# Kernel tuning notes

Hardware: AMD Instinct MI355X
Metric: run time of the kernel (lower is better)

The kernel has to match this reference:

```python
import jax, jax.numpy as jnp
import numpy as np

MAX_REL_POS = 16


def relative_position_ids(t, max_pos):
    r = jnp.arange(t)
    dist = jnp.clip(r[None, :] - r[:, None], -max_pos, max_pos)
    return dist + max_pos  # [T, T] in [0, 2*max_pos]


def setup_inputs():
    key = jax.random.key(0)
    ks = jax.random.split(key, 5)
    B, H, T, D = 2, 16, 1024, 64
    V = 2 * MAX_REL_POS + 1  # 33
    q = jax.random.normal(ks[0], (B, H, T, D), dtype=jnp.float32)
    k = jax.random.normal(ks[1], (B, H, T, D), dtype=jnp.float32)
    v = jax.random.normal(ks[2], (B, H, T, D), dtype=jnp.float32)
    embed_k = jax.random.normal(ks[3], (V, D), dtype=jnp.float32)
    embed_v = jax.random.normal(ks[4], (V, D), dtype=jnp.float32)
    mask = jnp.zeros((1, 1, T, T), dtype=jnp.float32)
    return {"q": q, "k": k, "v": v, "embed_k": embed_k, "embed_v": embed_v, "mask": mask}


def reference(q, k, v, embed_k, embed_v, mask):
    T = q.shape[2]
    D = k.shape[-1]
    rel = relative_position_ids(T, MAX_REL_POS)           # [T, T] int
    rel_k = embed_k[rel]                                   # [T, T, D]
    rel_v = embed_v[rel]                                   # [T, T, D]
    # QK^T plus relative-key term (matmul_with_relative_representations, transpose_b=True)
    logits = jnp.einsum('bhqd,bhkd->bhqk', q, k) + jnp.einsum('bhqd,qkd->bhqk', q, rel_k)
    logits = logits * (1.0 / jnp.sqrt(jnp.asarray(D, dtype=logits.dtype)))
    logits = logits + mask * (-1e9)
    attn = jax.nn.softmax(logits, axis=-1)                 # [B, H, T, T]
    out = jnp.einsum('bhqk,bhkd->bhqd', attn, v) + jnp.einsum('bhqk,qkd->bhqd', attn, rel_v)
    return out, attn
```

## Files before the change

### kernel.cpp

```cpp
#include <hip/hip_runtime.h>

#define BHN 32
#define T 1024
#define DD 64
#define TQ 16
#define PST 1032

typedef __attribute__((ext_vector_type(8))) __bf16 bf16x8;
typedef __attribute__((ext_vector_type(8))) unsigned short us8;
typedef __attribute__((ext_vector_type(4))) float f32x4;

struct alignas(16) U4 { unsigned a, b, c, d; };

__device__ __forceinline__ unsigned short f2bf(float x) {
  unsigned u = __builtin_bit_cast(unsigned, x);
  u += 0x7fffu + ((u >> 16) & 1u);
  return (unsigned short)(u >> 16);
}
__device__ __forceinline__ float bf2f(unsigned short h) {
  unsigned u = ((unsigned)h) << 16;
  return __builtin_bit_cast(float, u);
}
__device__ __forceinline__ bf16x8 ld_bf16x8(const unsigned short* p) {
  U4 u = *(const U4*)p;
  return __builtin_bit_cast(bf16x8, u);
}

__global__ __launch_bounds__(256) void prep_conv(
    const float* __restrict__ k, const float* __restrict__ v,
    unsigned short* __restrict__ kbf, unsigned short* __restrict__ vt)
{
  __shared__ float sT[64][65];
  const int bh = blockIdx.y;
  const int tb = blockIdx.x * 64;
  const int t = threadIdx.x;
  const size_t base = (size_t)bh * T * DD + (size_t)tb * DD;

  const float4* ksrc = (const float4*)(k + base);
  ushort4* kdst = (ushort4*)(kbf + base);
#pragma unroll
  for (int i = 0; i < 4; ++i) {
    int g = i * 256 + t;
    float4 f = ksrc[g];
    ushort4 u;
    u.x = f2bf(f.x); u.y = f2bf(f.y); u.z = f2bf(f.z); u.w = f2bf(f.w);
    kdst[g] = u;
  }

  const float* vsrc = v + base;
#pragma unroll
  for (int i = 0; i < 16; ++i) {
    int e = i * 256 + t;
    sT[e & 63][e >> 6] = vsrc[e];
  }
  __syncthreads();
  unsigned short* vdst = vt + (size_t)bh * DD * T + tb;
#pragma unroll
  for (int i = 0; i < 16; ++i) {
    int e = i * 256 + t;
    int dd = e >> 6, kk = e & 63;
    vdst[(size_t)dd * T + kk] = f2bf(sT[dd][kk]);
  }
}

__global__ __launch_bounds__(256, 4) void attn_main(
    const float* __restrict__ q, const unsigned short* __restrict__ kbf,
    const unsigned short* __restrict__ vt, const float* __restrict__ ek,
    const float* __restrict__ ev, const float* __restrict__ mask,
    float* __restrict__ out, float* __restrict__ attn)
{
  __shared__ unsigned short sP[TQ * PST];
  __shared__ float sQek[TQ][33];
  __shared__ float sDiag[TQ][31];
  __shared__ float sRS[4][TQ];
  __shared__ float sRB[4][TQ];
  __shared__ float sInv[TQ];
  __shared__ float sB0n[TQ];

  const int bh = blockIdx.y;
  const int qb = blockIdx.x * TQ;
  const int tid = threadIdx.x;
  const int wave = tid >> 6;
  const int lane = tid & 63;
  const int quad = lane >> 4;
  const int col = lane & 15;

  for (int i = tid; i < TQ * 31; i += 256) (&sDiag[0][0])[i] = 0.f;

  const float* qrows = q + (size_t)bh * T * DD + (size_t)qb * DD;
  for (int idx = tid; idx < TQ * 33; idx += 256) {
    int i = idx / 33;
    int r = idx - i * 33;
    const float4* qa = (const float4*)(qrows + i * DD);
    const float4* eb = (const float4*)(ek + r * DD);
    float acc = 0.f;
#pragma unroll
    for (int d4 = 0; d4 < 16; ++d4) {
      float4 a = qa[d4], b = eb[d4];
      acc += a.x * b.x + a.y * b.y + a.z * b.z + a.w * b.w;
    }
    sQek[i][r] = acc;
  }
  __syncthreads();

  bf16x8 aq0, aq1;
  {
    const float* qp = qrows + col * DD + quad * 8;
    float4 f0 = *(const float4*)(qp);
    float4 f1 = *(const float4*)(qp + 4);
    float4 f2 = *(const float4*)(qp + 32);
    float4 f3 = *(const float4*)(qp + 36);
    us8 u0, u1;
    u0[0] = f2bf(f0.x); u0[1] = f2bf(f0.y); u0[2] = f2bf(f0.z); u0[3] = f2bf(f0.w);
    u0[4] = f2bf(f1.x); u0[5] = f2bf(f1.y); u0[6] = f2bf(f1.z); u0[7] = f2bf(f1.w);
    u1[0] = f2bf(f2.x); u1[1] = f2bf(f2.y); u1[2] = f2bf(f2.z); u1[3] = f2bf(f2.w);
    u1[4] = f2bf(f3.x); u1[5] = f2bf(f3.y); u1[6] = f2bf(f3.z); u1[7] = f2bf(f3.w);
    aq0 = __builtin_bit_cast(bf16x8, u0);
    aq1 = __builtin_bit_cast(bf16x8, u1);
  }

  float regS[4] = {0.f, 0.f, 0.f, 0.f};
  float regB[4] = {0.f, 0.f, 0.f, 0.f};
  const unsigned short* kbh = kbf + (size_t)bh * T * DD;
  for (int it = 0; it < 16; ++it) {
    int kt = wave * 256 + it * 16;
    const unsigned short* kp = kbh + (size_t)(kt + col) * DD + quad * 8;
    bf16x8 bk0 = ld_bf16x8(kp);
    bf16x8 bk1 = ld_bf16x8(kp + 32);
    f32x4 acc = {0.f, 0.f, 0.f, 0.f};
    acc = __builtin_amdgcn_mfma_f32_16x16x32_bf16(aq0, bk0, acc, 0, 0, 0);
    acc = __builtin_amdgcn_mfma_f32_16x16x32_bf16(aq1, bk1, acc, 0, 0, 0);
    int kg = kt + col;
#pragma unroll
    for (int r = 0; r < 4; ++r) {
      int row = quad * 4 + r;
      int qg = qb + row;
      int dk = kg - qg;
      int rel = dk < -16 ? 0 : (dk > 16 ? 32 : dk + 16);
      float logit = (acc[r] + sQek[row][rel]) * 0.125f
                  + mask[(size_t)qg * T + kg] * (-1e9f);
      float p = __expf(fminf(logit, 80.f));
      sP[row * PST + kg] = f2bf(p);
      regS[r] += p;
      if (dk <= -16) regB[r] += p;
      if ((unsigned)(dk + 15) < 31u) sDiag[row][dk + 15] = p;
    }
  }

#pragma unroll
  for (int r = 0; r < 4; ++r) {
    float s = regS[r], b = regB[r];
#pragma unroll
    for (int off = 1; off < 16; off <<= 1) {
      s += __shfl_xor(s, off, 64);
      b += __shfl_xor(b, off, 64);
    }
    if (col == 0) { sRS[wave][quad * 4 + r] = s; sRB[wave][quad * 4 + r] = b; }
  }
  __syncthreads();
  if (tid < TQ) {
    float S = sRS[0][tid] + sRS[1][tid] + sRS[2][tid] + sRS[3][tid];
    float B0 = sRB[0][tid] + sRB[1][tid] + sRB[2][tid] + sRB[3][tid];
    float inv = 1.f / S;
    sInv[tid] = inv;
    sB0n[tid] = B0 * inv;
  }
  __syncthreads();

  float* attnq = attn + (size_t)bh * T * T + (size_t)qb * T;
#pragma unroll
  for (int i = 0; i < 16; ++i) {
    int e = i * 256 + tid;
    int row = e >> 8;
    int c4 = (e & 255) * 4;
    float inv = sInv[row];
    const unsigned short* pp = &sP[row * PST + c4];
    float4 o;
    o.x = bf2f(pp[0]) * inv;
    o.y = bf2f(pp[1]) * inv;
    o.z = bf2f(pp[2]) * inv;
    o.w = bf2f(pp[3]) * inv;
    *(float4*)(attnq + (size_t)row * T + c4) = o;
  }

  const unsigned short* vtw = vt + (size_t)bh * DD * T + (size_t)(wave * 16 + col) * T;
  f32x4 oacc = {0.f, 0.f, 0.f, 0.f};
  for (int kc = 0; kc < 32; ++kc) {
    bf16x8 ap = ld_bf16x8(&sP[col * PST + kc * 32 + quad * 8]);
    bf16x8 bv = ld_bf16x8(vtw + kc * 32 + quad * 8);
    oacc = __builtin_amdgcn_mfma_f32_16x16x32_bf16(ap, bv, oacc, 0, 0, 0);
  }

  const int dcol = wave * 16 + col;
  float ev0 = ev[dcol];
  float ev32 = ev[32 * DD + dcol];
  float invr[4], accv[4];
#pragma unroll
  for (int r = 0; r < 4; ++r) {
    int row = quad * 4 + r;
    float inv = sInv[row];
    invr[r] = inv;
    float sumd = 0.f;
#pragma unroll
    for (int j = 0; j < 31; ++j) sumd += sDiag[row][j];
    float b0 = sB0n[row];
    float b32 = 1.f - b0 - sumd * inv;
    accv[r] = oacc[r] * inv + b0 * ev0 + b32 * ev32;
  }
  for (int j = 0; j < 31; ++j) {
    float e = ev[(j + 1) * DD + dcol];
#pragma unroll
    for (int r = 0; r < 4; ++r)
      accv[r] += sDiag[quad * 4 + r][j] * invr[r] * e;
  }
  float* outp = out + (size_t)bh * T * DD + (size_t)qb * DD;
#pragma unroll
  for (int r = 0; r < 4; ++r)
    outp[(size_t)(quad * 4 + r) * DD + dcol] = accv[r];
}

extern "C" void kernel_launch(void* const* d_in, const int* in_sizes, int n_in,
                              void* d_out, int out_size, void* d_ws, size_t ws_size,
                              hipStream_t stream) {
  const float* q    = (const float*)d_in[0];
  const float* k    = (const float*)d_in[1];
  const float* v    = (const float*)d_in[2];
  const float* ek   = (const float*)d_in[3];
  const float* ev   = (const float*)d_in[4];
  const float* mask = (const float*)d_in[5];

  float* out  = (float*)d_out;
  float* attn = out + (size_t)BHN * T * DD;

  unsigned short* kbf = (unsigned short*)d_ws;
  unsigned short* vt  = kbf + (size_t)BHN * T * DD;

  dim3 pg(T / 64, BHN);
  prep_conv<<<pg, 256, 0, stream>>>(k, v, kbf, vt);

  dim3 g(T / TQ, BHN);
  attn_main<<<g, 256, 0, stream>>>(q, kbf, vt, ek, ev, mask, out, attn);
}
```

Measured before the change: 276.6 us.

## Vectorize prep conversion, prefetch K/mask, fast-path off-diagonal tiles, nontemporal attn stores

Rewrites prep_conv to use wider vector loads and stores for the K conversion and V transpose, and pads the shared tile. In the main kernel it software-prefetches the next K fragment and mask values, and adds a fast path for key tiles that lie entirely outside the relative-position band. It also moves the PV MFMA loop before the attention-probability write-out and writes attn with nontemporal stores. The aim is to cut scalar memory traffic and latency stalls, at the cost of more register pressure.

```diff
diff --git a/kernel.cpp b/kernel.cpp
--- a/kernel.cpp
+++ b/kernel.cpp
@@ -30,36 +30,48 @@
     const float* __restrict__ k, const float* __restrict__ v,
     unsigned short* __restrict__ kbf, unsigned short* __restrict__ vt)
 {
-  __shared__ float sT[64][65];
+  __shared__ float sT[64][66];
   const int bh = blockIdx.y;
   const int tb = blockIdx.x * 64;
   const int t = threadIdx.x;
   const size_t base = (size_t)bh * T * DD + (size_t)tb * DD;
 
   const float4* ksrc = (const float4*)(k + base);
-  ushort4* kdst = (ushort4*)(kbf + base);
+#pragma unroll
+  for (int i = 0; i < 2; ++i) {
+    int g = i * 256 + t;
+    float4 a = ksrc[g * 2], b = ksrc[g * 2 + 1];
+    us8 u;
+    u[0] = f2bf(a.x); u[1] = f2bf(a.y); u[2] = f2bf(a.z); u[3] = f2bf(a.w);
+    u[4] = f2bf(b.x); u[5] = f2bf(b.y); u[6] = f2bf(b.z); u[7] = f2bf(b.w);
+    *(us8*)(kbf + base + (size_t)g * 8) = u;
+  }
+
+  const float4* v4 = (const float4*)(v + base);
 #pragma unroll
   for (int i = 0; i < 4; ++i) {
     int g = i * 256 + t;
-    float4 f = ksrc[g];
-    ushort4 u;
-    u.x = f2bf(f.x); u.y = f2bf(f.y); u.z = f2bf(f.z); u.w = f2bf(f.w);
-    kdst[g] = u;
-  }
-
-  const float* vsrc = v + base;
-#pragma unroll
-  for (int i = 0; i < 16; ++i) {
-    int e = i * 256 + t;
-    sT[e & 63][e >> 6] = vsrc[e];
-  }
-  __syncthreads();
+    float4 x = v4[g];
+    int tl = g >> 4;
+    int d0 = (g & 15) * 4;
+    sT[d0][tl] = x.x; sT[d0 + 1][tl] = x.y; sT[d0 + 2][tl] = x.z; sT[d0 + 3][tl] = x.w;
+  }
+  __syncthreads();
+
   unsigned short* vdst = vt + (size_t)bh * DD * T + tb;
 #pragma unroll
-  for (int i = 0; i < 16; ++i) {
-    int e = i * 256 + t;
-    int dd = e >> 6, kk = e & 63;
-    vdst[(size_t)dd * T + kk] = f2bf(sT[dd][kk]);
+  for (int i = 0; i < 2; ++i) {
+    int item = i * 256 + t;
+    int dd = item >> 3;
+    int kk0 = (item & 7) * 8;
+    float2 x0 = *(const float2*)&sT[dd][kk0];
+    float2 x1 = *(const float2*)&sT[dd][kk0 + 2];
+    float2 x2 = *(const float2*)&sT[dd][kk0 + 4];
+    float2 x3 = *(const float2*)&sT[dd][kk0 + 6];
+    us8 u;
+    u[0] = f2bf(x0.x); u[1] = f2bf(x0.y); u[2] = f2bf(x1.x); u[3] = f2bf(x1.y);
+    u[4] = f2bf(x2.x); u[5] = f2bf(x2.y); u[6] = f2bf(x3.x); u[7] = f2bf(x3.y);
+    *(us8*)(vdst + (size_t)dd * T + kk0) = u;
   }
 }
 
@@ -101,7 +113,6 @@
     }
     sQek[i][r] = acc;
   }
-  __syncthreads();
 
   bf16x8 aq0, aq1;
   {
@@ -118,33 +129,71 @@
     aq0 = __builtin_bit_cast(bf16x8, u0);
     aq1 = __builtin_bit_cast(bf16x8, u1);
   }
+  __syncthreads();
 
   float regS[4] = {0.f, 0.f, 0.f, 0.f};
   float regB[4] = {0.f, 0.f, 0.f, 0.f};
   const unsigned short* kbh = kbf + (size_t)bh * T * DD;
+  const float* mrow = mask + (size_t)(qb + quad * 4) * T + col;
+
+  float qe0r[4], qe32r[4];
+#pragma unroll
+  for (int r = 0; r < 4; ++r) {
+    qe0r[r] = sQek[quad * 4 + r][0];
+    qe32r[r] = sQek[quad * 4 + r][32];
+  }
+
+  int kt0 = wave * 256;
+  const unsigned short* kp0 = kbh + (size_t)(kt0 + col) * DD + quad * 8;
+  bf16x8 bk0 = ld_bf16x8(kp0);
+  bf16x8 bk1 = ld_bf16x8(kp0 + 32);
+  float mv0 = mrow[kt0], mv1 = mrow[T + kt0], mv2 = mrow[2 * T + kt0], mv3 = mrow[3 * T + kt0];
+
   for (int it = 0; it < 16; ++it) {
-    int kt = wave * 256 + it * 16;
-    const unsigned short* kp = kbh + (size_t)(kt + col) * DD + quad * 8;
-    bf16x8 bk0 = ld_bf16x8(kp);
-    bf16x8 bk1 = ld_bf16x8(kp + 32);
+    const int ktc = wave * 256 + it * 16;
+    const int ktn = wave * 256 + ((it + 1) & 15) * 16;
+    const unsigned short* kpn = kbh + (size_t)(ktn + col) * DD + quad * 8;
+    bf16x8 nk0 = ld_bf16x8(kpn);
+    bf16x8 nk1 = ld_bf16x8(kpn + 32);
+    float nm0 = mrow[ktn], nm1 = mrow[T + ktn], nm2 = mrow[2 * T + ktn], nm3 = mrow[3 * T + ktn];
+
     f32x4 acc = {0.f, 0.f, 0.f, 0.f};
     acc = __builtin_amdgcn_mfma_f32_16x16x32_bf16(aq0, bk0, acc, 0, 0, 0);
     acc = __builtin_amdgcn_mfma_f32_16x16x32_bf16(aq1, bk1, acc, 0, 0, 0);
-    int kg = kt + col;
-#pragma unroll
-    for (int r = 0; r < 4; ++r) {
-      int row = quad * 4 + r;
-      int qg = qb + row;
-      int dk = kg - qg;
-      int rel = dk < -16 ? 0 : (dk > 16 ? 32 : dk + 16);
-      float logit = (acc[r] + sQek[row][rel]) * 0.125f
-                  + mask[(size_t)qg * T + kg] * (-1e9f);
-      float p = __expf(fminf(logit, 80.f));
-      sP[row * PST + kg] = f2bf(p);
-      regS[r] += p;
-      if (dk <= -16) regB[r] += p;
-      if ((unsigned)(dk + 15) < 31u) sDiag[row][dk + 15] = p;
+
+    const int kg = ktc + col;
+    unsigned short* spp = &sP[kg];
+    const float mv[4] = {mv0, mv1, mv2, mv3};
+    const int dkmax = ktc + 15 - qb;
+    const int dkmin = ktc - qb - 15;
+
+    if (dkmax < -16 || dkmin > 16) {
+      const bool low = dkmax < -16;
+#pragma unroll
+      for (int r = 0; r < 4; ++r) {
+        float qv = low ? qe0r[r] : qe32r[r];
+        float logit = fmaf(mv[r], -1e9f, (acc[r] + qv) * 0.125f);
+        float p = __expf(fminf(logit, 80.f));
+        spp[(quad * 4 + r) * PST] = f2bf(p);
+        regS[r] += p;
+        if (low) regB[r] += p;
+      }
+    } else {
+#pragma unroll
+      for (int r = 0; r < 4; ++r) {
+        int row = quad * 4 + r;
+        int dk = kg - (qb + row);
+        int rel = dk < -16 ? 0 : (dk > 16 ? 32 : dk + 16);
+        float logit = fmaf(mv[r], -1e9f, (acc[r] + sQek[row][rel]) * 0.125f);
+        float p = __expf(fminf(logit, 80.f));
+        spp[row * PST] = f2bf(p);
+        regS[r] += p;
+        if (dk <= -16) regB[r] += p;
+        if ((unsigned)(dk + 15) < 31u) sDiag[row][dk + 15] = p;
+      }
     }
+    bk0 = nk0; bk1 = nk1;
+    mv0 = nm0; mv1 = nm1; mv2 = nm2; mv3 = nm3;
   }
 
 #pragma unroll
@@ -165,30 +214,28 @@
     sInv[tid] = inv;
     sB0n[tid] = B0 * inv;
   }
-  __syncthreads();
-
-  float* attnq = attn + (size_t)bh * T * T + (size_t)qb * T;
-#pragma unroll
-  for (int i = 0; i < 16; ++i) {
-    int e = i * 256 + tid;
-    int row = e >> 8;
-    int c4 = (e & 255) * 4;
-    float inv = sInv[row];
-    const unsigned short* pp = &sP[row * PST + c4];
-    float4 o;
-    o.x = bf2f(pp[0]) * inv;
-    o.y = bf2f(pp[1]) * inv;
-    o.z = bf2f(pp[2]) * inv;
-    o.w = bf2f(pp[3]) * inv;
-    *(float4*)(attnq + (size_t)row * T + c4) = o;
-  }
-
-  const unsigned short* vtw = vt + (size_t)bh * DD * T + (size_t)(wave * 16 + col) * T;
+
+  const unsigned short* vtw = vt + (size_t)bh * DD * T + (size_t)(wave * 16 + col) * T + quad * 8;
   f32x4 oacc = {0.f, 0.f, 0.f, 0.f};
+#pragma unroll 4
   for (int kc = 0; kc < 32; ++kc) {
     bf16x8 ap = ld_bf16x8(&sP[col * PST + kc * 32 + quad * 8]);
-    bf16x8 bv = ld_bf16x8(vtw + kc * 32 + quad * 8);
+    bf16x8 bv = ld_bf16x8(vtw + kc * 32);
     oacc = __builtin_amdgcn_mfma_f32_16x16x32_bf16(ap, bv, oacc, 0, 0, 0);
+  }
+  __syncthreads();
+
+  float* attnq = attn + (size_t)bh * T * T + (size_t)qb * T;
+#pragma unroll 4
+  for (int i = 0; i < 16; ++i) {
+    float inv = sInv[i];
+    ushort4 u = *(const ushort4*)&sP[i * PST + tid * 4];
+    f32x4 o;
+    o[0] = bf2f(u.x) * inv;
+    o[1] = bf2f(u.y) * inv;
+    o[2] = bf2f(u.z) * inv;
+    o[3] = bf2f(u.w) * inv;
+    __builtin_nontemporal_store(o, (f32x4*)(attnq + (size_t)i * T + tid * 4));
   }
 
   const int dcol = wave * 16 + col;
```

After: 279.1 us. Within noise of the previous version (+0.9%).
